# Kernel tuning notes

Measured on AMD Instinct MI355X. Metric: run time of the kernel, lower is better.

The kernel has to match this reference:

```python
import jax, jax.numpy as jnp
import numpy as np
from jax import lax

B, N, S, K = 8, 4096, 1024, 32   # batch, points, npoint (FPS samples), nsample (ball query)
RADIUS = 0.15
ALPHA = 0.2                      # LeakyReLU negative slope
EPS = 1e-5                       # BatchNorm eps
MLP = [64, 64, 128]
D_IN = 6                         # per-point feature dim


def _index_points(p, idx):
    # p: [B, N, C]; idx: [B, ...] -> [B, ..., C]
    return jax.vmap(lambda pp, ii: pp[ii])(p, idx)


def _fps(xyz, npoint):
    # Farthest point sampling. Deterministic start at index 0 (original uses randint).
    b, n, _ = xyz.shape
    def step(carry, _):
        dist, far = carry
        c = xyz[jnp.arange(b), far]                    # [b,3] current centroid
        d = jnp.sum((xyz - c[:, None, :]) ** 2, -1)    # [b,n]
        dist = jnp.minimum(dist, d)
        return (dist, jnp.argmax(dist, -1).astype(jnp.int32)), far
    init = (jnp.full((b, n), 1e10, xyz.dtype), jnp.zeros((b,), jnp.int32))
    _, cent = lax.scan(step, init, None, length=npoint)
    return cent.T                                       # [b, npoint]


def _ball_query(radius, nsample, xyz, new_xyz):
    n = xyz.shape[1]
    # squared distances [B,S,N]
    sqr = (jnp.sum(new_xyz ** 2, -1)[:, :, None]
           + jnp.sum(xyz ** 2, -1)[:, None, :]
           - 2.0 * jnp.einsum('bsc,bnc->bsn', new_xyz, xyz))
    idx = jnp.where(sqr > radius * radius, n,
                    jnp.arange(n, dtype=jnp.int32)[None, None, :])
    idx = jnp.sort(idx, axis=-1)[:, :, :nsample]        # [B,S,K]
    return jnp.where(idx == n, idx[:, :, :1], idx)      # pad misses with first hit


def _mlp_bn_relu(x, w, b, g, be, m, v):
    # 1x1 Conv2d == linear on last axis; BatchNorm in eval mode with running stats.
    x = jnp.einsum('...c,oc->...o', x, w) + b
    x = g * (x - m) * lax.rsqrt(v + EPS) + be
    return jax.nn.relu(x)


def reference(xyz, points, w0, b0, g0, be0, m0, v0, w1, b1, g1, be1, m1, v1,
              w2, b2, g2, be2, m2, v2, a):
    params = [(w0, b0, g0, be0, m0, v0), (w1, b1, g1, be1, m1, v1),
              (w2, b2, g2, be2, m2, v2)]
    xyz_t = xyz.transpose(0, 2, 1)                      # [B,N,3]
    pts = points.transpose(0, 2, 1)                     # [B,N,D]

    fps_idx = _fps(xyz_t, S)                            # [B,S]
    new_xyz = _index_points(xyz_t, fps_idx)             # [B,S,3]
    idx = _ball_query(RADIUS, K, xyz_t, new_xyz)        # [B,S,K]
    grouped_xyz = _index_points(xyz_t, idx)             # [B,S,K,3]
    grouped_pts = _index_points(pts, idx)               # [B,S,K,D]
    fps_pts = _index_points(pts, fps_idx)               # [B,S,D]

    center = jnp.concatenate([new_xyz, fps_pts], -1)                       # [B,S,3+D]
    neigh = jnp.concatenate([grouped_xyz - new_xyz[:, :, None, :],
                             grouped_pts], -1)                             # [B,S,K,3+D]

    for (w, b, g, be, m, v) in params:
        center = _mlp_bn_relu(center, w, b, g, be, m, v)
        neigh = _mlp_bn_relu(neigh, w, b, g, be, m, v)

    # Graph attention: LeakyReLU scores, softmax over neighbors, weighted sum.
    dp = new_xyz[:, :, None, :] - grouped_xyz                              # [B,S,K,3]
    dh = center[:, :, None, :] - neigh                                     # [B,S,K,Dout]
    e = jax.nn.leaky_relu(jnp.concatenate([dp, dh], -1) @ a, ALPHA)        # [B,S,K,Dout]
    att = jax.nn.softmax(e, axis=2)                                        # over K
    out = jnp.sum(att * neigh, axis=2)                                     # [B,S,Dout]

    return new_xyz.transpose(0, 2, 1), out.transpose(0, 2, 1)              # [B,3,S],[B,Dout,S]


def setup_inputs() -> dict:
    key = jax.random.key(0)
    ks = jax.random.split(key, 32)
    inp = {
        'xyz': jax.random.uniform(ks[0], (B, 3, N), jnp.float32),
        'points': jax.random.normal(ks[1], (B, D_IN, N), jnp.float32),
    }
    last = 3 + D_IN
    j = 2
    for i, out_c in enumerate(MLP):
        scale = np.sqrt(2.0 / (last + out_c)).astype(np.float32)
        inp[f'w{i}'] = jax.random.normal(ks[j], (out_c, last), jnp.float32) * scale; j += 1
        inp[f'b{i}'] = jax.random.normal(ks[j], (out_c,), jnp.float32) * 0.01; j += 1
        inp[f'g{i}'] = 1.0 + 0.1 * jax.random.normal(ks[j], (out_c,), jnp.float32); j += 1
        inp[f'be{i}'] = 0.1 * jax.random.normal(ks[j], (out_c,), jnp.float32); j += 1
        inp[f'm{i}'] = 0.1 * jax.random.normal(ks[j], (out_c,), jnp.float32); j += 1
        inp[f'v{i}'] = 0.5 + jax.random.uniform(ks[j], (out_c,), jnp.float32); j += 1
        last = out_c
    inp['a'] = jax.random.normal(ks[j], (3 + MLP[-1], MLP[-1]), jnp.float32) * np.sqrt(2.0 / (3 + 2 * MLP[-1])).astype(np.float32)
    return inp


if __name__ == '__main__':
    o = reference(**setup_inputs())
    print(o[0].shape, o[1].shape)
```

## Files before the change

### kernel.cpp

```cpp
#include <hip/hip_runtime.h>

#define NB  8
#define NPT 4096
#define NS  1024
#define NK  32
#define DIN 6
#define QPB 32
#define MEGA_THREADS 512

#define OFF_A   0
#define OFF_W1  16768
#define OFF_W2  20864
#define OFF_W0  29056
#define OFF_H1  29632
#define OFF_H2  31808
#define OFF_U   33984
#define FLT_TOT 38208
#define SMEM_BYTES (FLT_TOT * 4)

__device__ __forceinline__ float bnrelu(float acc, const float* __restrict__ bb,
                                        const float* __restrict__ gg,
                                        const float* __restrict__ be,
                                        const float* __restrict__ mm,
                                        const float* __restrict__ vv, int oc) {
  float t = (acc + bb[oc]) - mm[oc];
  float val = gg[oc] * t * rsqrtf(vv[oc] + 1e-5f) + be[oc];
  return fmaxf(val, 0.0f);
}

__device__ __forceinline__ float wave64_max(float x) {
  const int NEG1 = 0xbf800000;
  int v;
  v = __builtin_amdgcn_update_dpp(NEG1, __float_as_int(x), 0x111, 0xf, 0xf, false);
  x = fmaxf(x, __int_as_float(v));
  v = __builtin_amdgcn_update_dpp(NEG1, __float_as_int(x), 0x112, 0xf, 0xf, false);
  x = fmaxf(x, __int_as_float(v));
  v = __builtin_amdgcn_update_dpp(NEG1, __float_as_int(x), 0x114, 0xf, 0xf, false);
  x = fmaxf(x, __int_as_float(v));
  v = __builtin_amdgcn_update_dpp(NEG1, __float_as_int(x), 0x118, 0xf, 0xf, false);
  x = fmaxf(x, __int_as_float(v));
  v = __builtin_amdgcn_update_dpp(NEG1, __float_as_int(x), 0x142, 0xa, 0xf, false);
  x = fmaxf(x, __int_as_float(v));
  v = __builtin_amdgcn_update_dpp(NEG1, __float_as_int(x), 0x143, 0xc, 0xf, false);
  x = fmaxf(x, __int_as_float(v));
  return __int_as_float(__builtin_amdgcn_readlane(__float_as_int(x), 63));
}

__global__ __launch_bounds__(512) void fps_kernel(const float* __restrict__ xyz,
                                                  int* __restrict__ fps_idx,
                                                  float* __restrict__ nxyz,
                                                  float* __restrict__ out0) {
  const int b = blockIdx.x;
  const int t = threadIdx.x;
  const int lane = t & 63, wid = t >> 6;
  const float* xb = xyz + (size_t)b * 3 * NPT;

  __shared__ float s_x[NPT], s_y[NPT], s_z[NPT];
  __shared__ __align__(16) float s_red[2][8][2];
  __shared__ float s_ox[NS], s_oy[NS], s_oz[NS];
  __shared__ int s_fi[NS];

  float px[8], py[8], pz[8], dist[8];
  const int base = t * 8;
#pragma unroll
  for (int j = 0; j < 8; ++j) {
    px[j] = xb[base + j];
    py[j] = xb[NPT + base + j];
    pz[j] = xb[2 * NPT + base + j];
    dist[j] = 1e10f;
  }
  for (int i = t; i < NPT; i += 512) {
    s_x[i] = xb[i];
    s_y[i] = xb[NPT + i];
    s_z[i] = xb[2 * NPT + i];
  }
  __syncthreads();

  int far = 0;
  float cx = xb[0], cy = xb[NPT], cz = xb[2 * NPT];

  for (int s = 0; s < NS; ++s) {
    if (t == 0) {
      s_ox[s] = cx; s_oy[s] = cy; s_oz[s] = cz; s_fi[s] = far;
    }
    float bv = -1.0f;
    int bi = 0;
#pragma unroll
    for (int j = 0; j < 8; ++j) {
      float dx = __fsub_rn(px[j], cx);
      float dy = __fsub_rn(py[j], cy);
      float dz = __fsub_rn(pz[j], cz);
      float d = __fadd_rn(__fadd_rn(__fmul_rn(dx, dx), __fmul_rn(dy, dy)),
                          __fmul_rn(dz, dz));
      float nd = fminf(dist[j], d);
      dist[j] = nd;
      bi = (nd > bv) ? (base + j) : bi;
      bv = fmaxf(bv, nd);
    }
    float mv = wave64_max(bv);
    unsigned long long mmask = __ballot(bv == mv);
    int src = __ffsll(mmask) - 1;
    int wi = __shfl(bi, src);

    const int p = s & 1;
    if (lane == 0) {
      s_red[p][wid][0] = mv;
      s_red[p][wid][1] = __int_as_float(wi);
    }
    __syncthreads();

    float4 q0 = *(const float4*)&s_red[p][0][0];
    float4 q1 = *(const float4*)&s_red[p][2][0];
    float4 q2 = *(const float4*)&s_red[p][4][0];
    float4 q3 = *(const float4*)&s_red[p][6][0];
    float va, vb, vc, vd; int ia, ib, ic, id;
    { bool g = q0.z > q0.x; va = g ? q0.z : q0.x;
      ia = g ? __float_as_int(q0.w) : __float_as_int(q0.y); }
    { bool g = q1.z > q1.x; vb = g ? q1.z : q1.x;
      ib = g ? __float_as_int(q1.w) : __float_as_int(q1.y); }
    { bool g = q2.z > q2.x; vc = g ? q2.z : q2.x;
      ic = g ? __float_as_int(q2.w) : __float_as_int(q2.y); }
    { bool g = q3.z > q3.x; vd = g ? q3.z : q3.x;
      id = g ? __float_as_int(q3.w) : __float_as_int(q3.y); }
    { bool g = vb > va; va = g ? vb : va; ia = g ? ib : ia; }
    { bool g = vd > vc; vc = g ? vd : vc; ic = g ? id : ic; }
    { bool g = vc > va; va = g ? vc : va; ia = g ? ic : ia; }
    far = ia;
    cx = s_x[far]; cy = s_y[far]; cz = s_z[far];
  }

  __syncthreads();
  for (int i = t; i < NS; i += 512) {
    float X = s_ox[i], Y = s_oy[i], Z = s_oz[i];
    out0[((size_t)b * 3 + 0) * NS + i] = X;
    out0[((size_t)b * 3 + 1) * NS + i] = Y;
    out0[((size_t)b * 3 + 2) * NS + i] = Z;
    nxyz[((size_t)b * NS + i) * 3 + 0] = X;
    nxyz[((size_t)b * NS + i) * 3 + 1] = Y;
    nxyz[((size_t)b * NS + i) * 3 + 2] = Z;
    fps_idx[b * NS + i] = s_fi[i];
  }
}

__global__ __launch_bounds__(64) void center_kernel(
    const float* __restrict__ points, const float* __restrict__ nxyz,
    const int* __restrict__ fps_idx,
    const float* __restrict__ w0, const float* __restrict__ b0,
    const float* __restrict__ g0, const float* __restrict__ be0,
    const float* __restrict__ m0, const float* __restrict__ v0,
    const float* __restrict__ w1, const float* __restrict__ b1,
    const float* __restrict__ g1, const float* __restrict__ be1,
    const float* __restrict__ m1, const float* __restrict__ v1,
    const float* __restrict__ w2, const float* __restrict__ b2,
    const float* __restrict__ g2, const float* __restrict__ be2,
    const float* __restrict__ m2, const float* __restrict__ v2,
    const float* __restrict__ a, float* __restrict__ ceA) {
  const int bs = blockIdx.x;
  const int b = bs >> 10;
  const int t = threadIdx.x;

  __shared__ float ci[9];
  __shared__ float ch1[64];
  __shared__ float ch2[64];
  __shared__ float ch3[128];

  if (t < 9) {
    ci[t] = (t < 3) ? nxyz[(size_t)bs * 3 + t]
                    : points[((size_t)b * DIN + (t - 3)) * NPT + fps_idx[bs]];
  }
  __syncthreads();
  {
    float acc = 0.f;
#pragma unroll
    for (int c = 0; c < 9; ++c) acc = fmaf(ci[c], w0[t * 9 + c], acc);
    ch1[t] = bnrelu(acc, b0, g0, be0, m0, v0, t);
  }
  __syncthreads();
  {
    float acc = 0.f;
#pragma unroll 8
    for (int c = 0; c < 64; ++c) acc = fmaf(ch1[c], w1[t * 64 + c], acc);
    ch2[t] = bnrelu(acc, b1, g1, be1, m1, v1, t);
  }
  __syncthreads();
  for (int oc = t; oc < 128; oc += 64) {
    float acc = 0.f;
#pragma unroll 8
    for (int c = 0; c < 64; ++c) acc = fmaf(ch2[c], w2[oc * 64 + c], acc);
    ch3[oc] = bnrelu(acc, b2, g2, be2, m2, v2, oc);
  }
  __syncthreads();
  for (int oc = t; oc < 128; oc += 64) {
    float acc = 0.f;
#pragma unroll 8
    for (int c = 0; c < 128; ++c) acc = fmaf(ch3[c], a[(3 + c) * 128 + oc], acc);
    ceA[(size_t)bs * 128 + oc] = acc;
  }
}

__global__ __launch_bounds__(256) void ballq_kernel(
    const float* __restrict__ xyz, const float* __restrict__ nxyz,
    float4* __restrict__ gq) {
  const int bs = blockIdx.x;
  const int b = bs >> 10;
  const int t = threadIdx.x;
  const int lane = t & 63;
  const int wid = t >> 6;

  __shared__ int s_widx[4][NK];
  __shared__ int s_wc[4];

  const float* xb = xyz + (size_t)b * 3 * NPT;
  const float cx = nxyz[(size_t)bs * 3 + 0];
  const float cy = nxyz[(size_t)bs * 3 + 1];
  const float cz = nxyz[(size_t)bs * 3 + 2];

  {
    const float R2 = (float)(0.15 * 0.15);
    float s2c = __fadd_rn(__fadd_rn(__fmul_rn(cx, cx), __fmul_rn(cy, cy)),
                          __fmul_rn(cz, cz));
    int wcnt = 0;
    for (int g = 0; g < 16; ++g) {
      int n = wid * 1024 + g * 64 + lane;
      float x = xb[n];
      float y = xb[NPT + n];
      float z = xb[2 * NPT + n];
      float pn2 = __fadd_rn(__fadd_rn(__fmul_rn(x, x), __fmul_rn(y, y)),
                            __fmul_rn(z, z));
      float dot = fmaf(cz, z, fmaf(cy, y, __fmul_rn(cx, x)));
      float sqr = __fsub_rn(__fadd_rn(s2c, pn2), __fmul_rn(2.0f, dot));
      bool hit = !(sqr > R2);
      unsigned long long mm = __ballot(hit);
      int pos = wcnt + __popcll(mm & ((1ull << lane) - 1ull));
      if (hit && pos < NK) s_widx[wid][pos] = n;
      wcnt += __popcll(mm);
      if (wcnt >= NK) break;
    }
    if (lane == 0) s_wc[wid] = (wcnt < NK) ? wcnt : NK;
  }
  __syncthreads();

  if (t < NK) {
    int c0 = s_wc[0], c1 = s_wc[1], c2 = s_wc[2], c3 = s_wc[3];
    int total = c0 + c1 + c2 + c3;
    int cc[4] = {c0, c1, c2, c3};
    int p = (t < total) ? t : 0;
    int w = 0;
    while (w < 3 && p >= cc[w]) { p -= cc[w]; ++w; }
    int n = s_widx[w][p];
    float gx = __fsub_rn(xb[n], cx);
    float gy = __fsub_rn(xb[NPT + n], cy);
    float gz = __fsub_rn(xb[2 * NPT + n], cz);
    gq[(size_t)bs * NK + t] = make_float4(gx, gy, gz, __int_as_float(n));
  }
}

__global__ __launch_bounds__(MEGA_THREADS) void mega_kernel(
    const float* __restrict__ points, const float* __restrict__ ceA,
    const float4* __restrict__ gq,
    const float* __restrict__ w0, const float* __restrict__ b0,
    const float* __restrict__ g0, const float* __restrict__ be0,
    const float* __restrict__ m0, const float* __restrict__ v0,
    const float* __restrict__ w1, const float* __restrict__ b1,
    const float* __restrict__ g1, const float* __restrict__ be1,
    const float* __restrict__ m1, const float* __restrict__ v1,
    const float* __restrict__ w2, const float* __restrict__ b2,
    const float* __restrict__ g2, const float* __restrict__ be2,
    const float* __restrict__ m2, const float* __restrict__ v2,
    const float* __restrict__ a, float* __restrict__ out1) {
  extern __shared__ float lds[];
  float* s_a  = lds + OFF_A;
  float* s_w1 = lds + OFF_W1;
  float* s_w2 = lds + OFF_W2;
  float* s_w0 = lds + OFF_W0;
  float* s_h1 = lds + OFF_H1;
  float* s_h2 = lds + OFF_H2;
  float* s_u  = lds + OFF_U;

  const int t = threadIdx.x;
  const int k = t & 31;
  const int g16 = t >> 5;
  const int kk = t & 15;
  const int gg = t >> 4;

  {
    const float4* srcA = (const float4*)a;
    float4* dstA = (float4*)s_a;
    for (int i = t; i < 4192; i += MEGA_THREADS) dstA[i] = srcA[i];
    const float4* src1 = (const float4*)w1;
    float4* dst1 = (float4*)s_w1;
    for (int i = t; i < 1024; i += MEGA_THREADS) dst1[i] = src1[i];
    const float4* src2 = (const float4*)w2;
    float4* dst2 = (float4*)s_w2;
    for (int i = t; i < 2048; i += MEGA_THREADS) dst2[i] = src2[i];
    for (int i = t; i < 576; i += MEGA_THREADS) s_w0[i] = w0[i];
  }
  __syncthreads();

  const int bs0 = blockIdx.x * QPB;

  float4 gv = gq[(size_t)bs0 * NK + k];
  float pts[6];
  {
    int n = __float_as_int(gv.w);
    const float* pb = points + (size_t)(bs0 >> 10) * DIN * NPT + n;
#pragma unroll
    for (int c = 0; c < 6; ++c) pts[c] = pb[(size_t)c * NPT];
  }

  for (int q = 0; q < QPB; ++q) {
    const int bs = bs0 + q;
    const int b = bs >> 10;
    const int s = bs & 1023;

    const int qn = (q + 1 < QPB) ? (q + 1) : q;
    const int bsn = bs0 + qn;
    float4 gv_next = gq[(size_t)bsn * NK + k];

    {
      float in0[9];
      in0[0] = gv.x; in0[1] = gv.y; in0[2] = gv.z;
#pragma unroll
      for (int c = 0; c < 6; ++c) in0[3 + c] = pts[c];
      int oc0 = g16 * 4;
      float acc[4];
#pragma unroll
      for (int j = 0; j < 4; ++j) {
        float a0 = 0.f;
#pragma unroll
        for (int c = 0; c < 9; ++c)
          a0 = fmaf(in0[c], s_w0[(oc0 + j) * 9 + c], a0);
        acc[j] = bnrelu(a0, b0, g0, be0, m0, v0, oc0 + j);
      }
      *(float4*)&s_h1[k * 68 + oc0] = make_float4(acc[0], acc[1], acc[2], acc[3]);
    }
    __syncthreads();

    float pts_next[6];
    {
      int nn = __float_as_int(gv_next.w);
      const float* pbn = points + (size_t)(bsn >> 10) * DIN * NPT + nn;
#pragma unroll
      for (int c = 0; c < 6; ++c) pts_next[c] = pbn[(size_t)c * NPT];
    }

    {
      int oc0 = gg * 2;
      float a0[2] = {0.f, 0.f}, a1[2] = {0.f, 0.f};
      const float4* row0 = (const float4*)&s_h1[kk * 68];
      const float4* row1 = (const float4*)&s_h1[(kk + 16) * 68];
#pragma unroll 4
      for (int c4 = 0; c4 < 16; ++c4) {
        float4 h0 = row0[c4];
        float4 h1 = row1[c4];
#pragma unroll
        for (int j = 0; j < 2; ++j) {
          float4 wv = *(const float4*)&s_w1[(oc0 + j) * 64 + c4 * 4];
          a0[j] = fmaf(h0.x, wv.x, a0[j]);
          a0[j] = fmaf(h0.y, wv.y, a0[j]);
          a0[j] = fmaf(h0.z, wv.z, a0[j]);
          a0[j] = fmaf(h0.w, wv.w, a0[j]);
          a1[j] = fmaf(h1.x, wv.x, a1[j]);
          a1[j] = fmaf(h1.y, wv.y, a1[j]);
          a1[j] = fmaf(h1.z, wv.z, a1[j]);
          a1[j] = fmaf(h1.w, wv.w, a1[j]);
        }
      }
#pragma unroll
      for (int j = 0; j < 2; ++j) {
        a0[j] = bnrelu(a0[j], b1, g1, be1, m1, v1, oc0 + j);
        a1[j] = bnrelu(a1[j], b1, g1, be1, m1, v1, oc0 + j);
      }
      s_h2[kk * 68 + oc0] = a0[0];
      s_h2[kk * 68 + oc0 + 1] = a0[1];
      s_h2[(kk + 16) * 68 + oc0] = a1[0];
      s_h2[(kk + 16) * 68 + oc0 + 1] = a1[1];
    }
    __syncthreads();

    {
      int oc0 = gg * 4;
      float a0[4] = {0.f, 0.f, 0.f, 0.f}, a1[4] = {0.f, 0.f, 0.f, 0.f};
      const float4* row0 = (const float4*)&s_h2[kk * 68];
      const float4* row1 = (const float4*)&s_h2[(kk + 16) * 68];
#pragma unroll 4
      for (int c4 = 0; c4 < 16; ++c4) {
        float4 h0 = row0[c4];
        float4 h1 = row1[c4];
#pragma unroll
        for (int j = 0; j < 4; ++j) {
          float4 wv = *(const float4*)&s_w2[(oc0 + j) * 64 + c4 * 4];
          a0[j] = fmaf(h0.x, wv.x, a0[j]);
          a0[j] = fmaf(h0.y, wv.y, a0[j]);
          a0[j] = fmaf(h0.z, wv.z, a0[j]);
          a0[j] = fmaf(h0.w, wv.w, a0[j]);
          a1[j] = fmaf(h1.x, wv.x, a1[j]);
          a1[j] = fmaf(h1.y, wv.y, a1[j]);
          a1[j] = fmaf(h1.z, wv.z, a1[j]);
          a1[j] = fmaf(h1.w, wv.w, a1[j]);
        }
      }
#pragma unroll
      for (int j = 0; j < 4; ++j) {
        a0[j] = bnrelu(a0[j], b2, g2, be2, m2, v2, oc0 + j);
        a1[j] = bnrelu(a1[j], b2, g2, be2, m2, v2, oc0 + j);
      }
      *(float4*)&s_u[kk * 132 + oc0] = make_float4(a0[0], a0[1], a0[2], a0[3]);
      *(float4*)&s_u[(kk + 16) * 132 + oc0] =
          make_float4(a1[0], a1[1], a1[2], a1[3]);
      if (t < NK) {
        s_u[t * 132 + 128] = gv.x;
        s_u[t * 132 + 129] = gv.y;
        s_u[t * 132 + 130] = gv.z;
        s_u[t * 132 + 131] = 0.f;
      }
    }
    __syncthreads();

    {
      int oc0 = gg * 4;
      float a0[4] = {0.f, 0.f, 0.f, 0.f}, a1[4] = {0.f, 0.f, 0.f, 0.f};
      const float4* urow0 = (const float4*)&s_u[kk * 132];
      const float4* urow1 = (const float4*)&s_u[(kk + 16) * 132];
      for (int r4 = 0; r4 < 33; ++r4) {
        float4 uv0 = urow0[r4];
        float4 uv1 = urow1[r4];
        int r = r4 * 4;
#pragma unroll
        for (int cc = 0; cc < 4; ++cc) {
          int rr = r + cc;
          int arow = (rr < 128) ? (rr + 3) : (rr - 128);
          float uc0 = (cc == 0) ? uv0.x : (cc == 1) ? uv0.y : (cc == 2) ? uv0.z : uv0.w;
          float uc1 = (cc == 0) ? uv1.x : (cc == 1) ? uv1.y : (cc == 2) ? uv1.z : uv1.w;
          float4 av = *(const float4*)&s_a[arow * 128 + oc0];
          a0[0] = fmaf(uc0, av.x, a0[0]);
          a0[1] = fmaf(uc0, av.y, a0[1]);
          a0[2] = fmaf(uc0, av.z, a0[2]);
          a0[3] = fmaf(uc0, av.w, a0[3]);
          a1[0] = fmaf(uc1, av.x, a1[0]);
          a1[1] = fmaf(uc1, av.y, a1[1]);
          a1[2] = fmaf(uc1, av.z, a1[2]);
          a1[3] = fmaf(uc1, av.w, a1[3]);
        }
      }

      float4 cv = *(const float4*)&ceA[(size_t)bs * 128 + oc0];
      float4 h0v = *(const float4*)&s_u[kk * 132 + oc0];
      float4 h1v = *(const float4*)&s_u[(kk + 16) * 132 + oc0];
      float ce[4] = {cv.x, cv.y, cv.z, cv.w};
      float h0[4] = {h0v.x, h0v.y, h0v.z, h0v.w};
      float h1[4] = {h1v.x, h1v.y, h1v.z, h1v.w};

      float* outb = out1 + (size_t)b * 128 * NS + s;
#pragma unroll
      for (int j = 0; j < 4; ++j) {
        float e0 = ce[j] - a0[j];
        float e1 = ce[j] - a1[j];
        e0 = (e0 >= 0.f) ? e0 : 0.2f * e0;
        e1 = (e1 >= 0.f) ? e1 : 0.2f * e1;
        float mx = fmaxf(e0, e1);
#pragma unroll
        for (int off = 8; off > 0; off >>= 1)
          mx = fmaxf(mx, __shfl_xor(mx, off));
        float p0 = expf(e0 - mx);
        float p1 = expf(e1 - mx);
        float num = p0 * h0[j] + p1 * h1[j];
        float den = p0 + p1;
#pragma unroll
        for (int off = 8; off > 0; off >>= 1) {
          num += __shfl_xor(num, off);
          den += __shfl_xor(den, off);
        }
        if (kk == 0) outb[(size_t)(oc0 + j) * NS] = num / den;
      }
    }

    gv = gv_next;
#pragma unroll
    for (int c = 0; c < 6; ++c) pts[c] = pts_next[c];
  }
}

extern "C" void kernel_launch(void* const* d_in, const int* in_sizes, int n_in,
                              void* d_out, int out_size, void* d_ws,
                              size_t ws_size, hipStream_t stream) {
  (void)in_sizes; (void)n_in; (void)out_size; (void)ws_size;
  const float* xyz = (const float*)d_in[0];
  const float* points = (const float*)d_in[1];
  const float* w0 = (const float*)d_in[2];
  const float* b0 = (const float*)d_in[3];
  const float* g0 = (const float*)d_in[4];
  const float* be0 = (const float*)d_in[5];
  const float* m0 = (const float*)d_in[6];
  const float* v0 = (const float*)d_in[7];
  const float* w1 = (const float*)d_in[8];
  const float* b1 = (const float*)d_in[9];
  const float* g1 = (const float*)d_in[10];
  const float* be1 = (const float*)d_in[11];
  const float* m1 = (const float*)d_in[12];
  const float* v1 = (const float*)d_in[13];
  const float* w2 = (const float*)d_in[14];
  const float* b2 = (const float*)d_in[15];
  const float* g2 = (const float*)d_in[16];
  const float* be2 = (const float*)d_in[17];
  const float* m2 = (const float*)d_in[18];
  const float* v2 = (const float*)d_in[19];
  const float* a = (const float*)d_in[20];

  float* out0 = (float*)d_out;
  float* out1 = out0 + (size_t)NB * 3 * NS;

  int* fps = (int*)d_ws;
  float* nxyz = (float*)((char*)d_ws + 32768);
  float* ceA = (float*)((char*)d_ws + 131072);
  float4* gq = (float4*)((char*)d_ws + 131072 + 4194304);

  hipFuncSetAttribute(reinterpret_cast<const void*>(mega_kernel),
                      hipFuncAttributeMaxDynamicSharedMemorySize, SMEM_BYTES);

  fps_kernel<<<NB, 512, 0, stream>>>(xyz, fps, nxyz, out0);
  ballq_kernel<<<NB * NS, 256, 0, stream>>>(xyz, nxyz, gq);
  center_kernel<<<NB * NS, 64, 0, stream>>>(points, nxyz, fps,
      w0, b0, g0, be0, m0, v0, w1, b1, g1, be1, m1, v1,
      w2, b2, g2, be2, m2, v2, a, ceA);
  mega_kernel<<<NB * NS / QPB, MEGA_THREADS, SMEM_BYTES, stream>>>(
      points, ceA, gq,
      w0, b0, g0, be0, m0, v0, w1, b1, g1, be1, m1, v1,
      w2, b2, g2, be2, m2, v2, a, out1);
}
```

Before: 1.132 ms.

## Carry winner coordinates through FPS reduction and use fewer, wider threads

The farthest-point-sampling kernel now runs 256 threads with 16 points each, loaded with float4 reads, instead of 512 threads with 8 points. Each thread and wave tracks the coordinates of its best candidate alongside the index, so the block reduction yields the next centroid directly. This removes the shared-memory copy of the point cloud and the dependent LDS load after every step's barrier, and halves the number of waves in the per-step reduction. In exchange each thread does twice the serial distance work and holds more registers per step.

```diff
diff --git a/kernel.cpp b/kernel.cpp
--- a/kernel.cpp
+++ b/kernel.cpp
@@ -46,35 +46,35 @@
   return __int_as_float(__builtin_amdgcn_readlane(__float_as_int(x), 63));
 }
 
-__global__ __launch_bounds__(512) void fps_kernel(const float* __restrict__ xyz,
-                                                  int* __restrict__ fps_idx,
-                                                  float* __restrict__ nxyz,
-                                                  float* __restrict__ out0) {
+__global__ __launch_bounds__(256, 1) void fps_kernel(
+    const float* __restrict__ xyz, int* __restrict__ fps_idx,
+    float* __restrict__ nxyz, float* __restrict__ out0) {
   const int b = blockIdx.x;
   const int t = threadIdx.x;
   const int lane = t & 63, wid = t >> 6;
   const float* xb = xyz + (size_t)b * 3 * NPT;
 
-  __shared__ float s_x[NPT], s_y[NPT], s_z[NPT];
-  __shared__ __align__(16) float s_red[2][8][2];
+  __shared__ __align__(16) float s_rv[2][4][4];
+  __shared__ int s_ri[2][4];
   __shared__ float s_ox[NS], s_oy[NS], s_oz[NS];
   __shared__ int s_fi[NS];
 
-  float px[8], py[8], pz[8], dist[8];
-  const int base = t * 8;
-#pragma unroll
-  for (int j = 0; j < 8; ++j) {
-    px[j] = xb[base + j];
-    py[j] = xb[NPT + base + j];
-    pz[j] = xb[2 * NPT + base + j];
-    dist[j] = 1e10f;
-  }
-  for (int i = t; i < NPT; i += 512) {
-    s_x[i] = xb[i];
-    s_y[i] = xb[NPT + i];
-    s_z[i] = xb[2 * NPT + i];
-  }
-  __syncthreads();
+  float px[16], py[16], pz[16], dist[16];
+  const int base = t * 16;
+#pragma unroll
+  for (int j4 = 0; j4 < 4; ++j4) {
+    float4 vx = *(const float4*)&xb[base + j4 * 4];
+    float4 vy = *(const float4*)&xb[NPT + base + j4 * 4];
+    float4 vz = *(const float4*)&xb[2 * NPT + base + j4 * 4];
+    px[j4 * 4 + 0] = vx.x; px[j4 * 4 + 1] = vx.y;
+    px[j4 * 4 + 2] = vx.z; px[j4 * 4 + 3] = vx.w;
+    py[j4 * 4 + 0] = vy.x; py[j4 * 4 + 1] = vy.y;
+    py[j4 * 4 + 2] = vy.z; py[j4 * 4 + 3] = vy.w;
+    pz[j4 * 4 + 0] = vz.x; pz[j4 * 4 + 1] = vz.y;
+    pz[j4 * 4 + 2] = vz.z; pz[j4 * 4 + 3] = vz.w;
+  }
+#pragma unroll
+  for (int j = 0; j < 16; ++j) dist[j] = 1e10f;
 
   int far = 0;
   float cx = xb[0], cy = xb[NPT], cz = xb[2 * NPT];
@@ -83,10 +83,11 @@
     if (t == 0) {
       s_ox[s] = cx; s_oy[s] = cy; s_oz[s] = cz; s_fi[s] = far;
     }
-    float bv = -1.0f;
+
+    float bv = -1.0f, bx = 0.f, by = 0.f, bz = 0.f;
     int bi = 0;
 #pragma unroll
-    for (int j = 0; j < 8; ++j) {
+    for (int j = 0; j < 16; ++j) {
       float dx = __fsub_rn(px[j], cx);
       float dy = __fsub_rn(py[j], cy);
       float dz = __fsub_rn(pz[j], cz);
@@ -94,43 +95,48 @@
                           __fmul_rn(dz, dz));
       float nd = fminf(dist[j], d);
       dist[j] = nd;
-      bi = (nd > bv) ? (base + j) : bi;
-      bv = fmaxf(bv, nd);
-    }
+      bool g = nd > bv;
+      bi = g ? (base + j) : bi;
+      bx = g ? px[j] : bx;
+      by = g ? py[j] : by;
+      bz = g ? pz[j] : bz;
+      bv = g ? nd : bv;
+    }
+
     float mv = wave64_max(bv);
     unsigned long long mmask = __ballot(bv == mv);
     int src = __ffsll(mmask) - 1;
     int wi = __shfl(bi, src);
+    float wx = __shfl(bx, src);
+    float wy = __shfl(by, src);
+    float wz = __shfl(bz, src);
 
     const int p = s & 1;
     if (lane == 0) {
-      s_red[p][wid][0] = mv;
-      s_red[p][wid][1] = __int_as_float(wi);
+      *(float4*)&s_rv[p][wid][0] = make_float4(mv, wx, wy, wz);
+      s_ri[p][wid] = wi;
     }
     __syncthreads();
 
-    float4 q0 = *(const float4*)&s_red[p][0][0];
-    float4 q1 = *(const float4*)&s_red[p][2][0];
-    float4 q2 = *(const float4*)&s_red[p][4][0];
-    float4 q3 = *(const float4*)&s_red[p][6][0];
-    float va, vb, vc, vd; int ia, ib, ic, id;
-    { bool g = q0.z > q0.x; va = g ? q0.z : q0.x;
-      ia = g ? __float_as_int(q0.w) : __float_as_int(q0.y); }
-    { bool g = q1.z > q1.x; vb = g ? q1.z : q1.x;
-      ib = g ? __float_as_int(q1.w) : __float_as_int(q1.y); }
-    { bool g = q2.z > q2.x; vc = g ? q2.z : q2.x;
-      ic = g ? __float_as_int(q2.w) : __float_as_int(q2.y); }
-    { bool g = q3.z > q3.x; vd = g ? q3.z : q3.x;
-      id = g ? __float_as_int(q3.w) : __float_as_int(q3.y); }
-    { bool g = vb > va; va = g ? vb : va; ia = g ? ib : ia; }
-    { bool g = vd > vc; vc = g ? vd : vc; ic = g ? id : ic; }
-    { bool g = vc > va; va = g ? vc : va; ia = g ? ic : ia; }
-    far = ia;
-    cx = s_x[far]; cy = s_y[far]; cz = s_z[far];
-  }
-
-  __syncthreads();
-  for (int i = t; i < NS; i += 512) {
+    float4 r0 = *(const float4*)&s_rv[p][0][0];
+    float4 r1 = *(const float4*)&s_rv[p][1][0];
+    float4 r2 = *(const float4*)&s_rv[p][2][0];
+    float4 r3 = *(const float4*)&s_rv[p][3][0];
+    int i0 = s_ri[p][0], i1 = s_ri[p][1], i2 = s_ri[p][2], i3 = s_ri[p][3];
+    bool g01 = r1.x > r0.x;
+    float4 w01 = g01 ? r1 : r0;
+    int j01 = g01 ? i1 : i0;
+    bool g23 = r3.x > r2.x;
+    float4 w23 = g23 ? r3 : r2;
+    int j23 = g23 ? i3 : i2;
+    bool gf = w23.x > w01.x;
+    float4 wf = gf ? w23 : w01;
+    far = gf ? j23 : j01;
+    cx = wf.y; cy = wf.z; cz = wf.w;
+  }
+
+  __syncthreads();
+  for (int i = t; i < NS; i += 256) {
     float X = s_ox[i], Y = s_oy[i], Z = s_oz[i];
     out0[((size_t)b * 3 + 0) * NS + i] = X;
     out0[((size_t)b * 3 + 1) * NS + i] = Y;
@@ -518,7 +524,7 @@
   hipFuncSetAttribute(reinterpret_cast<const void*>(mega_kernel),
                       hipFuncAttributeMaxDynamicSharedMemorySize, SMEM_BYTES);
 
-  fps_kernel<<<NB, 512, 0, stream>>>(xyz, fps, nxyz, out0);
+  fps_kernel<<<NB, 256, 0, stream>>>(xyz, fps, nxyz, out0);
   ballq_kernel<<<NB * NS, 256, 0, stream>>>(xyz, nxyz, gq);
   center_kernel<<<NB * NS, 64, 0, stream>>>(points, nxyz, fps,
       w0, b0, g0, be0, m0, v0, w1, b1, g1, be1, m1, v1,
```

Result: slower. 1.258 ms (+11.1%).
